# Kernel optimization log

Hardware: AMD Instinct MI355X
Metric: run time of the kernel (lower is better)

Reference implementation:

```python
import jax, jax.numpy as jnp
import numpy as np

IN_DIMS, CELL_DIMS, OUT_DIMS, T = 64, 128, 64, 256
BATCH = 4096


def _xavier(key, shape):
    fan_in, fan_out = shape
    limit = float(np.sqrt(6.0 / (fan_in + fan_out)))
    return jax.random.uniform(key, shape, jnp.float32, -limit, limit)


def setup_inputs() -> dict:
    key = jax.random.key(0)
    k_in, k_k, k_rk, k_b, k_dw, k_db = jax.random.split(key, 6)
    inputs = jax.random.normal(k_in, (BATCH, T, IN_DIMS), jnp.float32)
    kernel = _xavier(k_k, (IN_DIMS, 2 * CELL_DIMS))
    recurrent_kernel = _xavier(k_rk, (CELL_DIMS, 2 * CELL_DIMS))
    # bias: forget-gate half initialized to log(1 + (T-2)*U[0,1)), rest zeros
    u = jax.random.uniform(k_b, (CELL_DIMS,), jnp.float32)
    recurrent_bias = jnp.concatenate(
        [jnp.log(1.0 + (T - 1 - 1.0) * u), jnp.zeros((CELL_DIMS,), jnp.float32)])
    # nn.Linear(cell_dims, out_dims): uniform(-1/sqrt(cell), 1/sqrt(cell))
    bound = 1.0 / float(np.sqrt(CELL_DIMS))
    dense_w = jax.random.uniform(k_dw, (CELL_DIMS, OUT_DIMS), jnp.float32, -bound, bound)
    dense_b = jax.random.uniform(k_db, (OUT_DIMS,), jnp.float32, -bound, bound)
    return {"inputs": inputs, "kernel": kernel, "recurrent_kernel": recurrent_kernel,
            "recurrent_bias": recurrent_bias, "dense_w": dense_w, "dense_b": dense_b}


def reference(inputs, kernel, recurrent_kernel, recurrent_bias, dense_w, dense_b):
    B = inputs.shape[0]
    cell = recurrent_kernel.shape[0]
    # Precompute input projections for all timesteps: [B, T, 2*cell]
    zx = jnp.einsum('bti,ic->btc', inputs, kernel) + recurrent_bias

    def step(c_state, zx_t):
        z = zx_t + c_state @ recurrent_kernel  # h_state == c_state
        f = jax.nn.sigmoid(z[:, :cell])
        c = f * c_state + (1.0 - f) * jnp.tanh(z[:, cell:])
        return c, None

    c0 = jnp.zeros((B, cell), inputs.dtype)
    h_final, _ = jax.lax.scan(step, c0, jnp.swapaxes(zx, 0, 1))  # scan over T
    return h_final @ dense_w + dense_b
```

## Files before the change

### kernel.cpp

```cpp
#include <hip/hip_runtime.h>

#define BATCH 4096
#define T 256
#define IN 64
#define CELL 128
#define ZDIM 256
#define OUTD 64
#define M 16

using f32x4 = __attribute__((ext_vector_type(4))) float;
using f4    = __attribute__((ext_vector_type(4))) float;
using h16x8 = __attribute__((ext_vector_type(8))) _Float16;
using fp16x2 = __attribute__((ext_vector_type(2))) __fp16;
typedef unsigned int u32t;

union h8cast { h16x8 v; fp16x2 h[4]; };
union pkcast { fp16x2 h; u32t u; };

#define MFMA16(A, B, C) __builtin_amdgcn_mfma_f32_16x16x32_f16(A, B, C, 0, 0, 0)

#define GATEPK(I)                                                               \
  {                                                                             \
    float fgA = __builtin_amdgcn_rcpf(1.f + __builtin_amdgcn_exp2f(fa[I]));     \
    float thA = 1.f - 2.f * __builtin_amdgcn_rcpf(__builtin_amdgcn_exp2f(ga[I]) + 1.f); \
    float cnA = fgA * (cregA[I] - thA) + thA;                                   \
    float fgB = __builtin_amdgcn_rcpf(1.f + __builtin_amdgcn_exp2f(fb[I]));     \
    float thB = 1.f - 2.f * __builtin_amdgcn_rcpf(__builtin_amdgcn_exp2f(gb[I]) + 1.f); \
    float cnB = fgB * (cregB[I] - thB) + thB;                                   \
    cregA[I] = cnA; cregB[I] = cnB;                                             \
    pkcast pk_; pk_.h = __builtin_amdgcn_cvt_pkrtz(cnA, cnB);                   \
    *(u32t*)(cn_ + woPk[I]) = pk_.u;                                            \
  }

#define CVT8(D0, D1, S0, S1, S2, S3)                                            \
  {                                                                             \
    h8cast u0_, u1_;                                                            \
    u0_.h[0] = __builtin_amdgcn_cvt_pkrtz(S0[0], S0[1]);                        \
    u0_.h[1] = __builtin_amdgcn_cvt_pkrtz(S0[2], S0[3]);                        \
    u0_.h[2] = __builtin_amdgcn_cvt_pkrtz(S1[0], S1[1]);                        \
    u0_.h[3] = __builtin_amdgcn_cvt_pkrtz(S1[2], S1[3]);                        \
    u1_.h[0] = __builtin_amdgcn_cvt_pkrtz(S2[0], S2[1]);                        \
    u1_.h[1] = __builtin_amdgcn_cvt_pkrtz(S2[2], S2[3]);                        \
    u1_.h[2] = __builtin_amdgcn_cvt_pkrtz(S3[0], S3[1]);                        \
    u1_.h[3] = __builtin_amdgcn_cvt_pkrtz(S3[2], S3[3]);                        \
    D0 = u0_.v; D1 = u1_.v;                                                     \
  }

#define STEP(CUR, NXT, TT, P)                                                   \
  {                                                                             \
    const char* cb_ = cbuf[P];                                                  \
    h16x8 ca0 = *(const h16x8*)(cb_ + ro[0]);                                   \
    h16x8 ca1 = *(const h16x8*)(cb_ + ro[1]);                                   \
    h16x8 ca2 = *(const h16x8*)(cb_ + ro[2]);                                   \
    h16x8 ca3 = *(const h16x8*)(cb_ + ro[3]);                                   \
               \
    zxf##NXT##A = MFMA16(xa_##NXT##0, bA0, bqA);                                \
    zxf##NXT##B = MFMA16(xa_##NXT##0, bB0, bqB);                                \
    zxg##NXT##A = MFMA16(xa_##NXT##0, bC0, bqC);                                \
    zxg##NXT##B = MFMA16(xa_##NXT##0, bD0, bqD);                                \
    zxf##NXT##A = MFMA16(xa_##NXT##1, bA1, zxf##NXT##A);                        \
    zxf##NXT##B = MFMA16(xa_##NXT##1, bB1, zxf##NXT##B);                        \
    zxg##NXT##A = MFMA16(xa_##NXT##1, bC1, zxg##NXT##A);                        \
    zxg##NXT##B = MFMA16(xa_##NXT##1, bD1, zxg##NXT##B);                        \
                         \
    f32x4 fa = MFMA16(ca0, bA2, zxf##CUR##A);                                   \
    f32x4 fb = MFMA16(ca0, bB2, zxf##CUR##B);                                   \
    f32x4 ga = MFMA16(ca0, bC2, zxg##CUR##A);                                   \
    f32x4 gb = MFMA16(ca0, bD2, zxg##CUR##B);                                   \
    fa = MFMA16(ca1, bA3, fa); fb = MFMA16(ca1, bB3, fb);                       \
    ga = MFMA16(ca1, bC3, ga); gb = MFMA16(ca1, bD3, gb);                       \
    fa = MFMA16(ca2, bA4, fa); fb = MFMA16(ca2, bB4, fb);                       \
    ga = MFMA16(ca2, bC4, ga); gb = MFMA16(ca2, bD4, gb);                       \
    fa = MFMA16(ca3, bA5, fa); fb = MFMA16(ca3, bB5, fb);                       \
    ga = MFMA16(ca3, bC5, ga); gb = MFMA16(ca3, bD5, gb);                       \
             \
    CVT8(xa_##CUR##0, xa_##CUR##1, xr_##CUR##0, xr_##CUR##1, xr_##CUR##2, xr_##CUR##3) \
    {                                                                           \
      const int tn = ((TT) + 4) & (T - 1);                                      \
      const float* xp = xbase + (size_t)tn * IN;                                \
      xr_##CUR##0 = *(const f4*)(xp);                                           \
      xr_##CUR##1 = *(const f4*)(xp + 4);                                       \
      xr_##CUR##2 = *(const f4*)(xp + 32);                                      \
      xr_##CUR##3 = *(const f4*)(xp + 36);                                      \
    }                                                                           \
    char* cn_ = cbuf[(P) ^ 1];                                                  \
    GATEPK(0) GATEPK(1) GATEPK(2) GATEPK(3)                                     \
      \
    asm volatile("s_waitcnt lgkmcnt(0)\n\ts_barrier" ::: "memory");             \
  }

__global__ __launch_bounds__(256, 1)
void llrnn_f16(const float* __restrict__ in,
               const float* __restrict__ Km,
               const float* __restrict__ Rm,
               const float* __restrict__ bz,
               const float* __restrict__ Wd,
               const float* __restrict__ bd,
               float* __restrict__ out)
{
  __shared__ __align__(16) char cbuf[2][M * CELL * 2];
  __shared__ float cfin[M * CELL];

  const int tid = threadIdx.x;
  const int w = tid >> 6;
  const int l = tid & 63;
  const int q = l & 15;
  const int g = l >> 4;
  const int rb = blockIdx.x * M;
  const int colA = 32 * w + 2 * q;
  const int colB = colA + 1;

  {
    u32t* z0 = (u32t*)cbuf[0];
    z0[tid] = 0; z0[tid + 256] = 0; z0[tid + 512] = 0; z0[tid + 768] = 0;
  }

  const float SF = -1.44269504f;
  const float SG =  2.88539008f;

  h16x8 bA0,bA1,bA2,bA3,bA4,bA5, bB0,bB1,bB2,bB3,bB4,bB5,
        bC0,bC1,bC2,bC3,bC4,bC5, bD0,bD1,bD2,bD3,bD4,bD5;
#define LOADW(DST, COL, KT, SC)                                                 \
  {                                                                             \
    _Pragma("unroll") for (int e = 0; e < 8; ++e) {                             \
      const int krow = 32 * (KT) + 8 * g + e;                                   \
      const float* src = ((KT) < 2) ? (Km + (size_t)krow * ZDIM)                \
                                    : (Rm + (size_t)(krow - IN) * ZDIM);        \
      DST[e] = (_Float16)(src[COL] * (SC));                                     \
    }                                                                           \
  }
  LOADW(bA0,colA,0,SF) LOADW(bA1,colA,1,SF) LOADW(bA2,colA,2,SF)
  LOADW(bA3,colA,3,SF) LOADW(bA4,colA,4,SF) LOADW(bA5,colA,5,SF)
  LOADW(bB0,colB,0,SF) LOADW(bB1,colB,1,SF) LOADW(bB2,colB,2,SF)
  LOADW(bB3,colB,3,SF) LOADW(bB4,colB,4,SF) LOADW(bB5,colB,5,SF)
  LOADW(bC0,colA+CELL,0,SG) LOADW(bC1,colA+CELL,1,SG) LOADW(bC2,colA+CELL,2,SG)
  LOADW(bC3,colA+CELL,3,SG) LOADW(bC4,colA+CELL,4,SG) LOADW(bC5,colA+CELL,5,SG)
  LOADW(bD0,colB+CELL,0,SG) LOADW(bD1,colB+CELL,1,SG) LOADW(bD2,colB+CELL,2,SG)
  LOADW(bD3,colB+CELL,3,SG) LOADW(bD4,colB+CELL,4,SG) LOADW(bD5,colB+CELL,5,SG)
#undef LOADW
  asm volatile("" : "+v"(bA0),"+v"(bA1),"+v"(bA2),"+v"(bA3),"+v"(bA4),"+v"(bA5),
                    "+v"(bB0),"+v"(bB1),"+v"(bB2),"+v"(bB3),"+v"(bB4),"+v"(bB5),
                    "+v"(bC0),"+v"(bC1),"+v"(bC2),"+v"(bC3),"+v"(bC4),"+v"(bC5),
                    "+v"(bD0),"+v"(bD1),"+v"(bD2),"+v"(bD3),"+v"(bD4),"+v"(bD5));

  const float bA_ = bz[colA] * SF, bB_ = bz[colB] * SF;
  const float bC_ = bz[colA + CELL] * SG, bD_ = bz[colB + CELL] * SG;
  f32x4 bqA = {bA_, bA_, bA_, bA_};
  f32x4 bqB = {bB_, bB_, bB_, bB_};
  f32x4 bqC = {bC_, bC_, bC_, bC_};
  f32x4 bqD = {bD_, bD_, bD_, bD_};
  asm volatile("" : "+v"(bqA), "+v"(bqB), "+v"(bqC), "+v"(bqD));

  int ro[4];
#pragma unroll
  for (int ct = 0; ct < 4; ++ct)
    ro[ct] = q * 256 + 16 * ((4 * ct + g) ^ (q & 7));
  int woPk[4];
#pragma unroll
  for (int i = 0; i < 4; ++i) {
    const int r = 4 * g + i;
    woPk[i] = r * 256 + 16 * ((4 * w + (q >> 2)) ^ (r & 7)) + ((4 * q) & 15);
  }

  const float* xbase = in + (size_t)(rb + q) * T * IN + 8 * g;

  f4 xr_E0 = *(const f4*)(xbase);
  f4 xr_E1 = *(const f4*)(xbase + 4);
  f4 xr_E2 = *(const f4*)(xbase + 32);
  f4 xr_E3 = *(const f4*)(xbase + 36);
  f4 xr_O0 = *(const f4*)(xbase + IN);
  f4 xr_O1 = *(const f4*)(xbase + IN + 4);
  f4 xr_O2 = *(const f4*)(xbase + IN + 32);
  f4 xr_O3 = *(const f4*)(xbase + IN + 36);

  h16x8 xa_E0, xa_E1, xa_O0, xa_O1;
  CVT8(xa_E0, xa_E1, xr_E0, xr_E1, xr_E2, xr_E3)
  CVT8(xa_O0, xa_O1, xr_O0, xr_O1, xr_O2, xr_O3)

  f32x4 zxfEA, zxfEB, zxgEA, zxgEB, zxfOA, zxfOB, zxgOA, zxgOB;
  zxfEA = MFMA16(xa_E0, bA0, bqA);
  zxfEB = MFMA16(xa_E0, bB0, bqB);
  zxgEA = MFMA16(xa_E0, bC0, bqC);
  zxgEB = MFMA16(xa_E0, bD0, bqD);
  zxfEA = MFMA16(xa_E1, bA1, zxfEA);
  zxfEB = MFMA16(xa_E1, bB1, zxfEB);
  zxgEA = MFMA16(xa_E1, bC1, zxgEA);
  zxgEB = MFMA16(xa_E1, bD1, zxgEB);

  xr_E0 = *(const f4*)(xbase + 2 * IN);
  xr_E1 = *(const f4*)(xbase + 2 * IN + 4);
  xr_E2 = *(const f4*)(xbase + 2 * IN + 32);
  xr_E3 = *(const f4*)(xbase + 2 * IN + 36);
  xr_O0 = *(const f4*)(xbase + 3 * IN);
  xr_O1 = *(const f4*)(xbase + 3 * IN + 4);
  xr_O2 = *(const f4*)(xbase + 3 * IN + 32);
  xr_O3 = *(const f4*)(xbase + 3 * IN + 36);

  f32x4 cregA = {0.f, 0.f, 0.f, 0.f};
  f32x4 cregB = {0.f, 0.f, 0.f, 0.f};

  __syncthreads();

  for (int t = 0; t < T; t += 2) {
    STEP(E, O, t, 0)
    STEP(O, E, t + 1, 1)
  }

#pragma unroll
  for (int i = 0; i < 4; ++i) {
    cfin[(4 * g + i) * CELL + colA] = cregA[i];
    cfin[(4 * g + i) * CELL + colB] = cregB[i];
  }
  __syncthreads();

  const int o = tid & 63;
  const int rp = tid >> 6;
  float a0 = bd[o], a1 = bd[o], a2 = bd[o], a3 = bd[o];
#pragma unroll 4
  for (int k = 0; k < CELL; ++k) {
    const float wv = Wd[(size_t)k * OUTD + o];
    a0 += cfin[rp * CELL + k] * wv;
    a1 += cfin[(rp + 4) * CELL + k] * wv;
    a2 += cfin[(rp + 8) * CELL + k] * wv;
    a3 += cfin[(rp + 12) * CELL + k] * wv;
  }
  out[(size_t)(rb + rp) * OUTD + o] = a0;
  out[(size_t)(rb + rp + 4) * OUTD + o] = a1;
  out[(size_t)(rb + rp + 8) * OUTD + o] = a2;
  out[(size_t)(rb + rp + 12) * OUTD + o] = a3;
}

extern "C" void kernel_launch(void* const* d_in, const int* in_sizes, int n_in,
                              void* d_out, int out_size, void* d_ws, size_t ws_size,
                              hipStream_t stream) {
  const float* in  = (const float*)d_in[0];
  const float* Km  = (const float*)d_in[1];
  const float* Rm  = (const float*)d_in[2];
  const float* bz  = (const float*)d_in[3];
  const float* Wd  = (const float*)d_in[4];
  const float* bd  = (const float*)d_in[5];
  float* out = (float*)d_out;

  dim3 grid(BATCH / M);
  dim3 block(256);
  hipLaunchKernelGGL(llrnn_f16, grid, block, 0, stream,
                     in, Km, Rm, bz, Wd, bd, out);
}
```

Baseline: 149.4 us.

## Pre-barrier accumulate own-wave k-slice of recurrent matmul to shorten critical path

Each wave writes the 32 columns of the new c state it computes, then reads its own slice back from LDS before the barrier and issues the matching recurrent MFMAs early, because that slice needs no other wave's output. The remaining three k-slices are reordered per wave (w+1, w+2, w+3) and consumed after the barrier. This takes one quarter of the serial recurrent MFMA chain off the post-barrier critical path. In exchange it adds an LDS read of freshly written data before the barrier, which relies on the wave's own LDS write being visible to itself, and it slightly changes register pressure.

```diff
diff --git a/kernel.cpp b/kernel.cpp
--- a/kernel.cpp
+++ b/kernel.cpp
@@ -48,12 +48,12 @@
 
 #define STEP(CUR, NXT, TT, P)                                                   \
   {                                                                             \
+                             \
     const char* cb_ = cbuf[P];                                                  \
-    h16x8 ca0 = *(const h16x8*)(cb_ + ro[0]);                                   \
-    h16x8 ca1 = *(const h16x8*)(cb_ + ro[1]);                                   \
-    h16x8 ca2 = *(const h16x8*)(cb_ + ro[2]);                                   \
-    h16x8 ca3 = *(const h16x8*)(cb_ + ro[3]);                                   \
-               \
+    h16x8 ca1 = *(const h16x8*)(cb_ + ro1);                                     \
+    h16x8 ca2 = *(const h16x8*)(cb_ + ro2);                                     \
+    h16x8 ca3 = *(const h16x8*)(cb_ + ro3);                                     \
+                  \
     zxf##NXT##A = MFMA16(xa_##NXT##0, bA0, bqA);                                \
     zxf##NXT##B = MFMA16(xa_##NXT##0, bB0, bqB);                                \
     zxg##NXT##A = MFMA16(xa_##NXT##0, bC0, bqC);                                \
@@ -62,18 +62,16 @@
     zxf##NXT##B = MFMA16(xa_##NXT##1, bB1, zxf##NXT##B);                        \
     zxg##NXT##A = MFMA16(xa_##NXT##1, bC1, zxg##NXT##A);                        \
     zxg##NXT##B = MFMA16(xa_##NXT##1, bD1, zxg##NXT##B);                        \
-                         \
-    f32x4 fa = MFMA16(ca0, bA2, zxf##CUR##A);                                   \
-    f32x4 fb = MFMA16(ca0, bB2, zxf##CUR##B);                                   \
-    f32x4 ga = MFMA16(ca0, bC2, zxg##CUR##A);                                   \
-    f32x4 gb = MFMA16(ca0, bD2, zxg##CUR##B);                                   \
-    fa = MFMA16(ca1, bA3, fa); fb = MFMA16(ca1, bB3, fb);                       \
-    ga = MFMA16(ca1, bC3, ga); gb = MFMA16(ca1, bD3, gb);                       \
-    fa = MFMA16(ca2, bA4, fa); fb = MFMA16(ca2, bB4, fb);                       \
-    ga = MFMA16(ca2, bC4, ga); gb = MFMA16(ca2, bD4, gb);                       \
-    fa = MFMA16(ca3, bA5, fa); fb = MFMA16(ca3, bB5, fb);                       \
-    ga = MFMA16(ca3, bC5, ga); gb = MFMA16(ca3, bD5, gb);                       \
-             \
+           \
+    f32x4 fa = MFMA16(ca1, bRA1, l1fa);                                         \
+    f32x4 fb = MFMA16(ca1, bRB1, l1fb);                                         \
+    f32x4 ga = MFMA16(ca1, bRC1, l1ga);                                         \
+    f32x4 gb = MFMA16(ca1, bRD1, l1gb);                                         \
+    fa = MFMA16(ca2, bRA2, fa); fb = MFMA16(ca2, bRB2, fb);                     \
+    ga = MFMA16(ca2, bRC2, ga); gb = MFMA16(ca2, bRD2, gb);                     \
+    fa = MFMA16(ca3, bRA3, fa); fb = MFMA16(ca3, bRB3, fb);                     \
+    ga = MFMA16(ca3, bRC3, ga); gb = MFMA16(ca3, bRD3, gb);                     \
+                             \
     CVT8(xa_##CUR##0, xa_##CUR##1, xr_##CUR##0, xr_##CUR##1, xr_##CUR##2, xr_##CUR##3) \
     {                                                                           \
       const int tn = ((TT) + 4) & (T - 1);                                      \
@@ -83,9 +81,16 @@
       xr_##CUR##2 = *(const f4*)(xp + 32);                                      \
       xr_##CUR##3 = *(const f4*)(xp + 36);                                      \
     }                                                                           \
+                                           \
     char* cn_ = cbuf[(P) ^ 1];                                                  \
     GATEPK(0) GATEPK(1) GATEPK(2) GATEPK(3)                                     \
-      \
+     \
+    h16x8 caO = *(const h16x8*)((const char*)cbuf[(P) ^ 1] + ro0);              \
+    l1fa = MFMA16(caO, bRA0, zxf##NXT##A);                                      \
+    l1fb = MFMA16(caO, bRB0, zxf##NXT##B);                                      \
+    l1ga = MFMA16(caO, bRC0, zxg##NXT##A);                                      \
+    l1gb = MFMA16(caO, bRD0, zxg##NXT##B);                                      \
+         \
     asm volatile("s_waitcnt lgkmcnt(0)\n\ts_barrier" ::: "memory");             \
   }
 
@@ -118,30 +123,41 @@
   const float SF = -1.44269504f;
   const float SG =  2.88539008f;
 
-  h16x8 bA0,bA1,bA2,bA3,bA4,bA5, bB0,bB1,bB2,bB3,bB4,bB5,
-        bC0,bC1,bC2,bC3,bC4,bC5, bD0,bD1,bD2,bD3,bD4,bD5;
-#define LOADW(DST, COL, KT, SC)                                                 \
+  const int f1 = (w + 1) & 3, f2 = (w + 2) & 3, f3 = (w + 3) & 3;
+
+  h16x8 bA0,bA1, bB0,bB1, bC0,bC1, bD0,bD1;
+  h16x8 bRA0,bRA1,bRA2,bRA3, bRB0,bRB1,bRB2,bRB3,
+        bRC0,bRC1,bRC2,bRC3, bRD0,bRD1,bRD2,bRD3;
+#define LOADK(DST, COL, KT, SC)                                                 \
   {                                                                             \
     _Pragma("unroll") for (int e = 0; e < 8; ++e) {                             \
       const int krow = 32 * (KT) + 8 * g + e;                                   \
-      const float* src = ((KT) < 2) ? (Km + (size_t)krow * ZDIM)                \
-                                    : (Rm + (size_t)(krow - IN) * ZDIM);        \
-      DST[e] = (_Float16)(src[COL] * (SC));                                     \
+      DST[e] = (_Float16)(Km[(size_t)krow * ZDIM + (COL)] * (SC));              \
     }                                                                           \
   }
-  LOADW(bA0,colA,0,SF) LOADW(bA1,colA,1,SF) LOADW(bA2,colA,2,SF)
-  LOADW(bA3,colA,3,SF) LOADW(bA4,colA,4,SF) LOADW(bA5,colA,5,SF)
-  LOADW(bB0,colB,0,SF) LOADW(bB1,colB,1,SF) LOADW(bB2,colB,2,SF)
-  LOADW(bB3,colB,3,SF) LOADW(bB4,colB,4,SF) LOADW(bB5,colB,5,SF)
-  LOADW(bC0,colA+CELL,0,SG) LOADW(bC1,colA+CELL,1,SG) LOADW(bC2,colA+CELL,2,SG)
-  LOADW(bC3,colA+CELL,3,SG) LOADW(bC4,colA+CELL,4,SG) LOADW(bC5,colA+CELL,5,SG)
-  LOADW(bD0,colB+CELL,0,SG) LOADW(bD1,colB+CELL,1,SG) LOADW(bD2,colB+CELL,2,SG)
-  LOADW(bD3,colB+CELL,3,SG) LOADW(bD4,colB+CELL,4,SG) LOADW(bD5,colB+CELL,5,SG)
-#undef LOADW
-  asm volatile("" : "+v"(bA0),"+v"(bA1),"+v"(bA2),"+v"(bA3),"+v"(bA4),"+v"(bA5),
-                    "+v"(bB0),"+v"(bB1),"+v"(bB2),"+v"(bB3),"+v"(bB4),"+v"(bB5),
-                    "+v"(bC0),"+v"(bC1),"+v"(bC2),"+v"(bC3),"+v"(bC4),"+v"(bC5),
-                    "+v"(bD0),"+v"(bD1),"+v"(bD2),"+v"(bD3),"+v"(bD4),"+v"(bD5));
+#define LOADR(DST, COL, FJ, SC)                                                 \
+  {                                                                             \
+    _Pragma("unroll") for (int e = 0; e < 8; ++e) {                             \
+      const int krow = 32 * (FJ) + 8 * g + e;                                   \
+      DST[e] = (_Float16)(Rm[(size_t)krow * ZDIM + (COL)] * (SC));              \
+    }                                                                           \
+  }
+  LOADK(bA0,colA,0,SF) LOADK(bA1,colA,1,SF)
+  LOADK(bB0,colB,0,SF) LOADK(bB1,colB,1,SF)
+  LOADK(bC0,colA+CELL,0,SG) LOADK(bC1,colA+CELL,1,SG)
+  LOADK(bD0,colB+CELL,0,SG) LOADK(bD1,colB+CELL,1,SG)
+  LOADR(bRA0,colA,w,SF)  LOADR(bRA1,colA,f1,SF)  LOADR(bRA2,colA,f2,SF)  LOADR(bRA3,colA,f3,SF)
+  LOADR(bRB0,colB,w,SF)  LOADR(bRB1,colB,f1,SF)  LOADR(bRB2,colB,f2,SF)  LOADR(bRB3,colB,f3,SF)
+  LOADR(bRC0,colA+CELL,w,SG)  LOADR(bRC1,colA+CELL,f1,SG)  LOADR(bRC2,colA+CELL,f2,SG)  LOADR(bRC3,colA+CELL,f3,SG)
+  LOADR(bRD0,colB+CELL,w,SG)  LOADR(bRD1,colB+CELL,f1,SG)  LOADR(bRD2,colB+CELL,f2,SG)  LOADR(bRD3,colB+CELL,f3,SG)
+#undef LOADK
+#undef LOADR
+  asm volatile("" : "+v"(bA0),"+v"(bA1),"+v"(bB0),"+v"(bB1),
+                    "+v"(bC0),"+v"(bC1),"+v"(bD0),"+v"(bD1));
+  asm volatile("" : "+v"(bRA0),"+v"(bRA1),"+v"(bRA2),"+v"(bRA3),
+                    "+v"(bRB0),"+v"(bRB1),"+v"(bRB2),"+v"(bRB3),
+                    "+v"(bRC0),"+v"(bRC1),"+v"(bRC2),"+v"(bRC3),
+                    "+v"(bRD0),"+v"(bRD1),"+v"(bRD2),"+v"(bRD3));
 
   const float bA_ = bz[colA] * SF, bB_ = bz[colB] * SF;
   const float bC_ = bz[colA + CELL] * SG, bD_ = bz[colB + CELL] * SG;
@@ -151,10 +167,10 @@
   f32x4 bqD = {bD_, bD_, bD_, bD_};
   asm volatile("" : "+v"(bqA), "+v"(bqB), "+v"(bqC), "+v"(bqD));
 
-  int ro[4];
-#pragma unroll
-  for (int ct = 0; ct < 4; ++ct)
-    ro[ct] = q * 256 + 16 * ((4 * ct + g) ^ (q & 7));
+  const int ro0 = q * 256 + 16 * ((4 * w  + g) ^ (q & 7));
+  const int ro1 = q * 256 + 16 * ((4 * f1 + g) ^ (q & 7));
+  const int ro2 = q * 256 + 16 * ((4 * f2 + g) ^ (q & 7));
+  const int ro3 = q * 256 + 16 * ((4 * f3 + g) ^ (q & 7));
   int woPk[4];
 #pragma unroll
   for (int i = 0; i < 4; ++i) {
@@ -200,6 +216,15 @@
   f32x4 cregB = {0.f, 0.f, 0.f, 0.f};
 
   __syncthreads();
+
+  f32x4 l1fa, l1fb, l1ga, l1gb;
+  {
+    h16x8 caO = *(const h16x8*)((const char*)cbuf[0] + ro0);
+    l1fa = MFMA16(caO, bRA0, zxfEA);
+    l1fb = MFMA16(caO, bRB0, zxfEB);
+    l1ga = MFMA16(caO, bRC0, zxgEA);
+    l1gb = MFMA16(caO, bRD0, zxgEB);
+  }
 
   for (int t = 0; t < T; t += 2) {
     STEP(E, O, t, 0)
```

New measurement: 158.3 us. 5.9% more time.
